# Optimization experiments

Measured on AMD Instinct MI355X. Metric: run time of the kernel, lower is better.

Reference implementation:

```python
import jax, jax.numpy as jnp
import numpy as np

NUM_CLUSTERS = 512
EMBED_DIM = 256
BATCH = 65536
ALPHA = 0.05

def setup_inputs() -> dict:
    key = jax.random.key(0)
    k1, k2 = jax.random.split(key)
    embeddings = jax.random.normal(k1, (BATCH, EMBED_DIM), dtype=jnp.float32)
    # torch.randn centers drawn inside forward; materialized here for determinism
    centers = jax.random.normal(k2, (NUM_CLUSTERS, EMBED_DIM), dtype=jnp.float32)
    return {"embeddings": embeddings, "centers": centers}

def reference(embeddings, centers):
    # the broadcast difference, without the huge [N, K, D] intermediate).
    x_sq = jnp.sum(embeddings * embeddings, axis=1, keepdims=True)      # [N, 1]
    c_sq = jnp.sum(centers * centers, axis=1)[None, :]                  # [1, K]
    cross = embeddings @ centers.T                                      # [N, K]
    distances = jnp.sqrt(jnp.maximum(x_sq + c_sq - 2.0 * cross, 0.0))   # [N, K]
    cluster_assignments = jnp.argmin(distances, axis=1)                 # [N] int
    # gather distance to assigned (nearest) center
    cluster_loss = jnp.take_along_axis(
        distances, cluster_assignments[:, None], axis=1)[:, 0]          # [N]
    kmeans_loss = jnp.mean(cluster_loss)
    return kmeans_loss * ALPHA
```

## Files before the change

kernel.cpp:

```cpp
#include <hip/hip_runtime.h>
#include <hip/hip_bf16.h>

#define NROWS 65536
#define DIM   256
#define KC    512
#define ALPHA 0.05f

#define BM   64
#define SLD  264

typedef __attribute__((ext_vector_type(8))) short bf16x8;
typedef __attribute__((ext_vector_type(4))) float f32x4;

static __device__ __forceinline__ unsigned short f2bf(float f) {
    union { __hip_bfloat16 h; unsigned short u; } c;
    c.h = __float2bfloat16(f);
    return c.u;
}
static __device__ __forceinline__ float bf2f(unsigned short u) {
    union { unsigned short u; __hip_bfloat16 h; } c;
    c.u = u;
    return __bfloat162float(c.h);
}

__global__ void prep_centers(const float* __restrict__ centers,
                             float* __restrict__ csqh,
                             uint4* __restrict__ cbf2,
                             float* __restrict__ out) {
    const int t = threadIdx.x;
    const int r = blockIdx.x * 8 + (t >> 5);
    const int e = t & 31;
    const float4* cv = reinterpret_cast<const float4*>(centers);
    float4 v0 = cv[r * 64 + e * 2];
    float4 v1 = cv[r * 64 + e * 2 + 1];
    float s = v0.x * v0.x + v0.y * v0.y + v0.z * v0.z + v0.w * v0.w
            + v1.x * v1.x + v1.y * v1.y + v1.z * v1.z + v1.w * v1.w;
    unsigned short o[8];
    o[0] = f2bf(v0.x); o[1] = f2bf(v0.y); o[2] = f2bf(v0.z); o[3] = f2bf(v0.w);
    o[4] = f2bf(v1.x); o[5] = f2bf(v1.y); o[6] = f2bf(v1.z); o[7] = f2bf(v1.w);
    const int ch = r >> 6, w = (r >> 4) & 3, m = r & 15;
    const int kk = e >> 2, q = e & 3, l = q * 16 + m;
    cbf2[(((ch * 4 + w) * 8) + kk) * 64 + l] = *reinterpret_cast<uint4*>(o);
    #pragma unroll
    for (int off = 16; off; off >>= 1) s += __shfl_xor(s, off, 64);
    if (e == 0) csqh[r] = 0.5f * s;
    if (blockIdx.x == 0 && t == 0) out[0] = 0.f;
}

__global__ __launch_bounds__(256, 2) void kmeans_main(
    const float* __restrict__ emb,
    const uint4* __restrict__ cbf2,
    const float* __restrict__ csqh_g,
    float* __restrict__ out) {
    __shared__ unsigned short sA[BM * SLD];
    __shared__ float xsq_s[BM];
    __shared__ float rowmax_s[4][BM];

    const int t = threadIdx.x;
    const int w = t >> 6;
    const int lane = t & 63;
    const int m = lane & 15;
    const int q = lane >> 4;
    const int row0 = blockIdx.x * BM;

    const float4* embv = reinterpret_cast<const float4*>(emb + (size_t)row0 * DIM);
    #pragma unroll
    for (int i = 0; i < 16; ++i) {
        int f = t + 256 * i;
        int r = f >> 6;
        int c4 = f & 63;
        float4 v = embv[r * 64 + c4];
        ushort4 o;
        o.x = f2bf(v.x); o.y = f2bf(v.y); o.z = f2bf(v.z); o.w = f2bf(v.w);
        *reinterpret_cast<ushort4*>(&sA[r * SLD + c4 * 4]) = o;
    }
    __syncthreads();

    {
        int r = w * 16 + (lane >> 2);
        int qq = lane & 3;
        const ushort4* p = reinterpret_cast<const ushort4*>(&sA[r * SLD + qq * 64]);
        float s = 0.f;
        #pragma unroll
        for (int j = 0; j < 16; ++j) {
            ushort4 u = p[j];
            float a = bf2f(u.x), b = bf2f(u.y), c = bf2f(u.z), d = bf2f(u.w);
            s += a * a + b * b + c * c + d * d;
        }
        s += __shfl_xor(s, 1, 64);
        s += __shfl_xor(s, 2, 64);
        if (qq == 0) xsq_s[r] = s;
    }

    bf16x8 afr[4][8];
    #pragma unroll
    for (int rt = 0; rt < 4; ++rt)
        #pragma unroll
        for (int k = 0; k < 8; ++k)
            afr[rt][k] = *reinterpret_cast<const bf16x8*>(
                &sA[(rt * 16 + m) * SLD + k * 32 + q * 8]);

    float c2h[8];
    #pragma unroll
    for (int ch = 0; ch < 8; ++ch) c2h[ch] = csqh_g[ch * 64 + w * 16 + m];

    float maxv[4][4];
    #pragma unroll
    for (int rt = 0; rt < 4; ++rt)
        #pragma unroll
        for (int rg = 0; rg < 4; ++rg) maxv[rt][rg] = -1e30f;

    const bf16x8* cb2 = reinterpret_cast<const bf16x8*>(cbf2);

    bf16x8 bcur[8];
    #pragma unroll
    for (int kk = 0; kk < 8; ++kk)
        bcur[kk] = cb2[((0 * 4 + w) * 8 + kk) * 64 + lane];

    #pragma unroll
    for (int ch = 0; ch < 8; ++ch) {
        bf16x8 bnxt[8];
        if (ch < 7) {
            #pragma unroll
            for (int kk = 0; kk < 8; ++kk)
                bnxt[kk] = cb2[(((ch + 1) * 4 + w) * 8 + kk) * 64 + lane];
        }
        const float ci = -c2h[ch];
        f32x4 acc[4];
        #pragma unroll
        for (int rt = 0; rt < 4; ++rt) acc[rt] = (f32x4){ci, ci, ci, ci};
        #pragma unroll
        for (int kk = 0; kk < 8; ++kk)
            #pragma unroll
            for (int rt = 0; rt < 4; ++rt)
                acc[rt] = __builtin_amdgcn_mfma_f32_16x16x32_bf16(
                    afr[rt][kk], bcur[kk], acc[rt], 0, 0, 0);
        #pragma unroll
        for (int rt = 0; rt < 4; ++rt)
            #pragma unroll
            for (int rg = 0; rg < 4; ++rg)
                maxv[rt][rg] = fmaxf(maxv[rt][rg], acc[rt][rg]);
        if (ch < 7) {
            #pragma unroll
            for (int kk = 0; kk < 8; ++kk) bcur[kk] = bnxt[kk];
        }
    }

    #pragma unroll
    for (int rt = 0; rt < 4; ++rt)
        #pragma unroll
        for (int rg = 0; rg < 4; ++rg) {
            float v = maxv[rt][rg];
            v = fmaxf(v, __shfl_xor(v, 1, 64));
            v = fmaxf(v, __shfl_xor(v, 2, 64));
            v = fmaxf(v, __shfl_xor(v, 4, 64));
            v = fmaxf(v, __shfl_xor(v, 8, 64));
            if (m == 0) rowmax_s[w][rt * 16 + q * 4 + rg] = v;
        }
    __syncthreads();

    if (t < 64) {
        float M = fmaxf(fmaxf(rowmax_s[0][t], rowmax_s[1][t]),
                        fmaxf(rowmax_s[2][t], rowmax_s[3][t]));
        float d = sqrtf(fmaxf(xsq_s[t] - 2.f * M, 0.f));
        #pragma unroll
        for (int off = 1; off < 64; off <<= 1) d += __shfl_xor(d, off, 64);
        if (t == 0) atomicAdd(out, d * (ALPHA / (float)NROWS));
    }
}

extern "C" void kernel_launch(void* const* d_in, const int* in_sizes, int n_in,
                              void* d_out, int out_size, void* d_ws, size_t ws_size,
                              hipStream_t stream) {
    const float* emb     = (const float*)d_in[0];
    const float* centers = (const float*)d_in[1];
    float* out = (float*)d_out;

    float* csqh = (float*)d_ws;
    uint4* cbf2 = (uint4*)((char*)d_ws + 2048);

    prep_centers<<<dim3(KC / 8), dim3(256), 0, stream>>>(centers, csqh, cbf2, out);
    kmeans_main<<<dim3(NROWS / BM), dim3(256), 0, stream>>>(emb, cbf2, csqh, out);
}
```

Measured before the change: 118.7 us.

## Load embedding fragments directly from global into registers and split waves by center half

The LDS staging of embeddings is removed. Each wave now loads its MFMA A fragments straight from global memory, converting to bf16 and computing the fp32 squared norms in registers. Waves are arranged as 2 row groups × 2 center halves, and each wave streams 16 center tiles. Launch bounds rise to 4 blocks per CU to raise occupancy. The catch is that each wave re-reads center tiles from L2 with less register-level reuse, and the global loads are less coalesced (strided per lane).

```diff
diff --git a/kernel.cpp b/kernel.cpp
--- a/kernel.cpp
+++ b/kernel.cpp
@@ -6,9 +6,6 @@
 #define KC    512
 #define ALPHA 0.05f
 
-#define BM   64
-#define SLD  264
-
 typedef __attribute__((ext_vector_type(8))) short bf16x8;
 typedef __attribute__((ext_vector_type(4))) float f32x4;
 
@@ -16,11 +13,6 @@
     union { __hip_bfloat16 h; unsigned short u; } c;
     c.h = __float2bfloat16(f);
     return c.u;
-}
-static __device__ __forceinline__ float bf2f(unsigned short u) {
-    union { unsigned short u; __hip_bfloat16 h; } c;
-    c.u = u;
-    return __bfloat162float(c.h);
 }
 
 __global__ void prep_centers(const float* __restrict__ centers,
@@ -38,116 +30,100 @@
     unsigned short o[8];
     o[0] = f2bf(v0.x); o[1] = f2bf(v0.y); o[2] = f2bf(v0.z); o[3] = f2bf(v0.w);
     o[4] = f2bf(v1.x); o[5] = f2bf(v1.y); o[6] = f2bf(v1.z); o[7] = f2bf(v1.w);
-    const int ch = r >> 6, w = (r >> 4) & 3, m = r & 15;
+    const int t16 = r >> 4, m = r & 15;
     const int kk = e >> 2, q = e & 3, l = q * 16 + m;
-    cbf2[(((ch * 4 + w) * 8) + kk) * 64 + l] = *reinterpret_cast<uint4*>(o);
+    cbf2[(t16 * 8 + kk) * 64 + l] = *reinterpret_cast<uint4*>(o);
     #pragma unroll
     for (int off = 16; off; off >>= 1) s += __shfl_xor(s, off, 64);
     if (e == 0) csqh[r] = 0.5f * s;
     if (blockIdx.x == 0 && t == 0) out[0] = 0.f;
 }
 
-__global__ __launch_bounds__(256, 2) void kmeans_main(
+__global__ __launch_bounds__(256, 4) void kmeans_main(
     const float* __restrict__ emb,
     const uint4* __restrict__ cbf2,
     const float* __restrict__ csqh_g,
     float* __restrict__ out) {
-    __shared__ unsigned short sA[BM * SLD];
-    __shared__ float xsq_s[BM];
-    __shared__ float rowmax_s[4][BM];
+    __shared__ float xsq_s[64];
+    __shared__ float rowmax_s[2][64];
 
     const int t = threadIdx.x;
     const int w = t >> 6;
     const int lane = t & 63;
     const int m = lane & 15;
     const int q = lane >> 4;
-    const int row0 = blockIdx.x * BM;
+    const int g = w >> 1;
+    const int h = w & 1;
+    const int r0 = blockIdx.x * 64 + g * 32;
 
-    const float4* embv = reinterpret_cast<const float4*>(emb + (size_t)row0 * DIM);
+    bf16x8 afr[2][8];
+    float xp[2];
     #pragma unroll
-    for (int i = 0; i < 16; ++i) {
-        int f = t + 256 * i;
-        int r = f >> 6;
-        int c4 = f & 63;
-        float4 v = embv[r * 64 + c4];
-        ushort4 o;
-        o.x = f2bf(v.x); o.y = f2bf(v.y); o.z = f2bf(v.z); o.w = f2bf(v.w);
-        *reinterpret_cast<ushort4*>(&sA[r * SLD + c4 * 4]) = o;
+    for (int rt = 0; rt < 2; ++rt) {
+        float s = 0.f;
+        const float* rowp = emb + (size_t)(r0 + rt * 16 + m) * DIM;
+        #pragma unroll
+        for (int kk = 0; kk < 8; ++kk) {
+            const float4* p = reinterpret_cast<const float4*>(rowp + kk * 32 + q * 8);
+            float4 v0 = p[0], v1 = p[1];
+            s += v0.x * v0.x + v0.y * v0.y + v0.z * v0.z + v0.w * v0.w
+               + v1.x * v1.x + v1.y * v1.y + v1.z * v1.z + v1.w * v1.w;
+            bf16x8 a;
+            a[0] = (short)f2bf(v0.x); a[1] = (short)f2bf(v0.y);
+            a[2] = (short)f2bf(v0.z); a[3] = (short)f2bf(v0.w);
+            a[4] = (short)f2bf(v1.x); a[5] = (short)f2bf(v1.y);
+            a[6] = (short)f2bf(v1.z); a[7] = (short)f2bf(v1.w);
+            afr[rt][kk] = a;
+        }
+        xp[rt] = s;
     }
-    __syncthreads();
-
-    {
-        int r = w * 16 + (lane >> 2);
-        int qq = lane & 3;
-        const ushort4* p = reinterpret_cast<const ushort4*>(&sA[r * SLD + qq * 64]);
-        float s = 0.f;
-        #pragma unroll
-        for (int j = 0; j < 16; ++j) {
-            ushort4 u = p[j];
-            float a = bf2f(u.x), b = bf2f(u.y), c = bf2f(u.z), d = bf2f(u.w);
-            s += a * a + b * b + c * c + d * d;
-        }
-        s += __shfl_xor(s, 1, 64);
-        s += __shfl_xor(s, 2, 64);
-        if (qq == 0) xsq_s[r] = s;
+    #pragma unroll
+    for (int rt = 0; rt < 2; ++rt) {
+        xp[rt] += __shfl_xor(xp[rt], 16, 64);
+        xp[rt] += __shfl_xor(xp[rt], 32, 64);
+        if (h == 0 && q == 0) xsq_s[g * 32 + rt * 16 + m] = xp[rt];
     }
 
-    bf16x8 afr[4][8];
+    float maxv[2][4];
     #pragma unroll
-    for (int rt = 0; rt < 4; ++rt)
-        #pragma unroll
-        for (int k = 0; k < 8; ++k)
-            afr[rt][k] = *reinterpret_cast<const bf16x8*>(
-                &sA[(rt * 16 + m) * SLD + k * 32 + q * 8]);
-
-    float c2h[8];
-    #pragma unroll
-    for (int ch = 0; ch < 8; ++ch) c2h[ch] = csqh_g[ch * 64 + w * 16 + m];
-
-    float maxv[4][4];
-    #pragma unroll
-    for (int rt = 0; rt < 4; ++rt)
+    for (int rt = 0; rt < 2; ++rt)
         #pragma unroll
         for (int rg = 0; rg < 4; ++rg) maxv[rt][rg] = -1e30f;
 
-    const bf16x8* cb2 = reinterpret_cast<const bf16x8*>(cbf2);
+    #pragma unroll 2
+    for (int ct = 0; ct < 16; ++ct) {
+        const int t16 = h * 16 + ct;
+        const float ci = -csqh_g[t16 * 16 + m];
+        const uint4* bp = cbf2 + t16 * 8 * 64 + lane;
 
-    bf16x8 bcur[8];
-    #pragma unroll
-    for (int kk = 0; kk < 8; ++kk)
-        bcur[kk] = cb2[((0 * 4 + w) * 8 + kk) * 64 + lane];
-
-    #pragma unroll
-    for (int ch = 0; ch < 8; ++ch) {
-        bf16x8 bnxt[8];
-        if (ch < 7) {
-            #pragma unroll
-            for (int kk = 0; kk < 8; ++kk)
-                bnxt[kk] = cb2[(((ch + 1) * 4 + w) * 8 + kk) * 64 + lane];
+        f32x4 acc0 = {ci, ci, ci, ci};
+        f32x4 acc1 = {ci, ci, ci, ci};
+        bf16x8 bfr[4];
+        #pragma unroll
+        for (int kk = 0; kk < 4; ++kk)
+            bfr[kk] = *reinterpret_cast<const bf16x8*>(bp + kk * 64);
+        #pragma unroll
+        for (int kk = 0; kk < 4; ++kk) {
+            acc0 = __builtin_amdgcn_mfma_f32_16x16x32_bf16(afr[0][kk], bfr[kk], acc0, 0, 0, 0);
+            acc1 = __builtin_amdgcn_mfma_f32_16x16x32_bf16(afr[1][kk], bfr[kk], acc1, 0, 0, 0);
         }
-        const float ci = -c2h[ch];
-        f32x4 acc[4];
         #pragma unroll
-        for (int rt = 0; rt < 4; ++rt) acc[rt] = (f32x4){ci, ci, ci, ci};
+        for (int kk = 0; kk < 4; ++kk)
+            bfr[kk] = *reinterpret_cast<const bf16x8*>(bp + (kk + 4) * 64);
         #pragma unroll
-        for (int kk = 0; kk < 8; ++kk)
-            #pragma unroll
-            for (int rt = 0; rt < 4; ++rt)
-                acc[rt] = __builtin_amdgcn_mfma_f32_16x16x32_bf16(
-                    afr[rt][kk], bcur[kk], acc[rt], 0, 0, 0);
+        for (int kk = 0; kk < 4; ++kk) {
+            acc0 = __builtin_amdgcn_mfma_f32_16x16x32_bf16(afr[0][kk + 4], bfr[kk], acc0, 0, 0, 0);
+            acc1 = __builtin_amdgcn_mfma_f32_16x16x32_bf16(afr[1][kk + 4], bfr[kk], acc1, 0, 0, 0);
+        }
         #pragma unroll
-        for (int rt = 0; rt < 4; ++rt)
-            #pragma unroll
-            for (int rg = 0; rg < 4; ++rg)
-                maxv[rt][rg] = fmaxf(maxv[rt][rg], acc[rt][rg]);
-        if (ch < 7) {
-            #pragma unroll
-            for (int kk = 0; kk < 8; ++kk) bcur[kk] = bnxt[kk];
+        for (int rg = 0; rg < 4; ++rg) {
+            maxv[0][rg] = fmaxf(maxv[0][rg], acc0[rg]);
+            maxv[1][rg] = fmaxf(maxv[1][rg], acc1[rg]);
         }
     }
 
     #pragma unroll
-    for (int rt = 0; rt < 4; ++rt)
+    for (int rt = 0; rt < 2; ++rt)
         #pragma unroll
         for (int rg = 0; rg < 4; ++rg) {
             float v = maxv[rt][rg];
@@ -155,13 +131,12 @@
             v = fmaxf(v, __shfl_xor(v, 2, 64));
             v = fmaxf(v, __shfl_xor(v, 4, 64));
             v = fmaxf(v, __shfl_xor(v, 8, 64));
-            if (m == 0) rowmax_s[w][rt * 16 + q * 4 + rg] = v;
+            if (m == 0) rowmax_s[h][g * 32 + rt * 16 + q * 4 + rg] = v;
         }
     __syncthreads();
 
     if (t < 64) {
-        float M = fmaxf(fmaxf(rowmax_s[0][t], rowmax_s[1][t]),
-                        fmaxf(rowmax_s[2][t], rowmax_s[3][t]));
+        float M = fmaxf(rowmax_s[0][t], rowmax_s[1][t]);
         float d = sqrtf(fmaxf(xsq_s[t] - 2.f * M, 0.f));
         #pragma unroll
         for (int off = 1; off < 64; off <<= 1) d += __shfl_xor(d, off, 64);
@@ -180,5 +155,5 @@
     uint4* cbf2 = (uint4*)((char*)d_ws + 2048);
 
     prep_centers<<<dim3(KC / 8), dim3(256), 0, stream>>>(centers, csqh, cbf2, out);
-    kmeans_main<<<dim3(NROWS / BM), dim3(256), 0, stream>>>(emb, cbf2, csqh, out);
+    kmeans_main<<<dim3(NROWS / 64), dim3(256), 0, stream>>>(emb, cbf2, csqh, out);
 }
```

After: 146.8 us. 23.7% more time.
